# Kernel tuning notes

Hardware: AMD Instinct MI355X
Metric: run time of the kernel (lower is better)

The kernel has to match this reference:

```python
import jax, jax.numpy as jnp
import numpy as np

B, S, D, H = 2, 2048, 1024, 16
DEPTH = D // H
NEG = -1e9

def setup_inputs() -> dict:
    key = jax.random.key(0)
    k = jax.random.split(key, 4)
    return {
        "token_inputs": jax.random.normal(k[0], (B, S, D), dtype=jnp.float32),
        "mask": jnp.zeros((B, 1, 1, S), dtype=jnp.float32),
        "W_qkv": jax.random.normal(k[1], (D, 3 * D), dtype=jnp.float32) * 0.02,
        "b_qkv": jnp.zeros((3 * D,), dtype=jnp.float32),
        "W_out": jax.random.normal(k[2], (D, D), dtype=jnp.float32) * 0.02,
        "b_out": jnp.zeros((D,), dtype=jnp.float32),
    }

def reference(token_inputs, mask, W_qkv, b_qkv, W_out, b_out):
    # fused QKV projection
    qkv = token_inputs @ W_qkv + b_qkv                       # [B,S,3D]
    q, k, v = jnp.split(qkv, 3, axis=-1)                     # [B,S,D] each
    # split heads -> [B,H,S,depth]
    split = lambda x: x.reshape(B, S, H, DEPTH).transpose(0, 2, 1, 3)
    q, k, v = split(q), split(k), split(v)
    # causal additive mask: 0 on/below diagonal, -1e9 above
    causal = (1.0 - jnp.tril(jnp.ones((S, S), dtype=jnp.float32))) * NEG
    full_mask = mask + causal                                # [B,1,S,S]
    # scaled dot-product attention
    scores = jnp.einsum('bhqd,bhkd->bhqk', q, k) / jnp.sqrt(jnp.float32(DEPTH))
    scores = scores + full_mask
    attn = jax.nn.softmax(scores, axis=-1)                   # [B,H,S,S]
    ctx = jnp.einsum('bhqk,bhkd->bhqd', attn, v)             # [B,H,S,depth]
    # merge heads and final projection
    ctx = ctx.transpose(0, 2, 1, 3).reshape(B, S, D)
    return ctx @ W_out + b_out
```

## Files before the change

kernel.cpp:

```cpp
#include <hip/hip_runtime.h>
#include <hip/hip_bf16.h>

#define B_ 2
#define S_ 2048
#define D_ 1024
#define H_ 16
#define DEPTH_ 64

typedef __attribute__((ext_vector_type(4))) float f32x4;
typedef __attribute__((ext_vector_type(16))) float f32x16;
typedef __attribute__((ext_vector_type(8))) short bf16x8;
typedef const __attribute__((address_space(1))) unsigned int gu32;
typedef __attribute__((address_space(3))) unsigned int lu32;

__device__ __forceinline__ void gload_lds16(const void* g, void* l) {
  __builtin_amdgcn_global_load_lds((gu32*)g, (lu32*)l, 16, 0, 0);
}

__device__ __forceinline__ short f2bf(float f) {
  union { float f; unsigned u; } v; v.f = f;
  return (short)((v.u + 0x7FFFu + ((v.u >> 16) & 1u)) >> 16);
}
__device__ __forceinline__ unsigned pk2(float lo, float hi) {
  unsigned r;
  asm("v_cvt_pk_bf16_f32 %0, %1, %2" : "=v"(r) : "v"(lo), "v"(hi));
  return r;
}

__global__ __launch_bounds__(256) void cast_kernel(const float* __restrict__ in,
                                                   short* __restrict__ out, int n4) {
  int i = blockIdx.x * 256 + threadIdx.x;
  if (i < n4) {
    const float4 v = reinterpret_cast<const float4*>(in)[i];
    short2 a, b;
    *reinterpret_cast<unsigned*>(&a) = pk2(v.x, v.y);
    *reinterpret_cast<unsigned*>(&b) = pk2(v.z, v.w);
    reinterpret_cast<short4*>(out)[i] = make_short4(a.x, a.y, b.x, b.y);
  }
}

__global__ __launch_bounds__(256) void transpose_cast_kernel(const float* __restrict__ W,
                                                             short* __restrict__ WT,
                                                             int K, int N) {
  __shared__ short tile[32][33];
  int n0 = blockIdx.x * 32, k0 = blockIdx.y * 32;
  int tx = threadIdx.x, ty = threadIdx.y;
#pragma unroll
  for (int j = 0; j < 4; ++j)
    tile[ty + 8 * j][tx] = f2bf(W[(size_t)(k0 + ty + 8 * j) * N + n0 + tx]);
  __syncthreads();
#pragma unroll
  for (int j = 0; j < 4; ++j)
    WT[(size_t)(n0 + ty + 8 * j) * K + k0 + tx] = tile[tx][ty + 8 * j];
}

template <int EPI, int BM>
__global__ __launch_bounds__(512) void gemm_bt_kernel(
    const short* __restrict__ A, const short* __restrict__ BT,
    const float* __restrict__ bias,
    short* __restrict__ Qh, short* __restrict__ Kh, short* __restrict__ VTt,
    float* __restrict__ Out, int M, int N, int K) {
  constexpr int MI = BM / 64;
  constexpr int ASZ = BM * 32;
  constexpr int BSZ = 128 * 32;
  __shared__ short smem[2 * ASZ + 2 * BSZ];
  const int bm = blockIdx.y * BM, bn = blockIdx.x * 128;
  const int tid = threadIdx.x;
  const int w = tid >> 6, lane = tid & 63;
  const int wr = w >> 1, wc = w & 1;
  const int lr = lane & 15, lg = lane >> 4;
  const int s_r = lane >> 2, s_c = (lane & 3) * 8;
  f32x4 acc[MI][4] = {};
  const int nk = K >> 5;

  auto stage = [&](int buf, int kt) {
    short* Asb = smem + (buf ? ASZ : 0);
    short* Bsb = smem + 2 * ASZ + (buf ? BSZ : 0);
    if (BM == 128 || w < 4)
      gload_lds16(&A[(size_t)(bm + 16 * w + s_r) * K + kt * 32 + s_c], &Asb[16 * w * 32]);
    gload_lds16(&BT[(size_t)(bn + 16 * w + s_r) * K + kt * 32 + s_c], &Bsb[16 * w * 32]);
  };

  stage(0, 0);
  __syncthreads();
  int cur = 0;
  for (int kt = 0; kt < nk; ++kt) {
    if (kt + 1 < nk) stage(cur ^ 1, kt + 1);
    const short* Asb = smem + (cur ? ASZ : 0);
    const short* Bsb = smem + 2 * ASZ + (cur ? BSZ : 0);
    bf16x8 af[MI], bfr[4];
#pragma unroll
    for (int mi = 0; mi < MI; ++mi)
      af[mi] = *reinterpret_cast<const bf16x8*>(&Asb[((BM / 4) * wr + 16 * mi + lr) * 32 + 8 * lg]);
#pragma unroll
    for (int ni = 0; ni < 4; ++ni)
      bfr[ni] = *reinterpret_cast<const bf16x8*>(&Bsb[(64 * wc + 16 * ni + lr) * 32 + 8 * lg]);
#pragma unroll
    for (int mi = 0; mi < MI; ++mi)
#pragma unroll
      for (int ni = 0; ni < 4; ++ni)
        acc[mi][ni] = __builtin_amdgcn_mfma_f32_16x16x32_bf16(af[mi], bfr[ni], acc[mi][ni], 0, 0, 0);
    __syncthreads();
    cur ^= 1;
  }

  if constexpr (EPI == 0) {
    if (bn >= 2 * D_) {
      __syncthreads();
      short* vt = smem;
#pragma unroll
      for (int mi = 0; mi < MI; ++mi)
#pragma unroll
        for (int ni = 0; ni < 4; ++ni)
#pragma unroll
          for (int r = 0; r < 4; r += 2) {
            int row_local = (BM / 4) * wr + 16 * mi + 4 * lg + r;
            int col_local = 64 * wc + 16 * ni + lr;
            float bv = bias[bn + col_local];
            unsigned u = pk2(acc[mi][ni][r] + bv, acc[mi][ni][r + 1] + bv);
            int rsw = row_local ^ ((col_local & 7) << 3);
            *reinterpret_cast<unsigned*>(&vt[col_local * 128 + rsw]) = u;
          }
      __syncthreads();
      const int b = bm >> 11, sbase = bm & (S_ - 1);
#pragma unroll
      for (int p = 0; p < 4; ++p) {
        int slot = 512 * p + tid;
        int vrow = slot >> 4, seg = slot & 15;
        int dd_col = bn - 2 * D_ + vrow;
        int hh = dd_col >> 6, dd = dd_col & 63;
        int csw = (seg * 8) ^ ((vrow & 7) << 3);
        short* dst = &VTt[((size_t)(b * H_ + hh) * DEPTH_ + dd) * S_ + sbase + seg * 8];
        *reinterpret_cast<bf16x8*>(dst) = *reinterpret_cast<const bf16x8*>(&vt[vrow * 128 + csw]);
      }
    } else {
#pragma unroll
      for (int mi = 0; mi < MI; ++mi)
#pragma unroll
        for (int ni = 0; ni < 4; ++ni)
#pragma unroll
          for (int r = 0; r < 4; ++r) {
            int row = bm + (BM / 4) * wr + 16 * mi + 4 * lg + r;
            int col = bn + 64 * wc + 16 * ni + lr;
            float v = acc[mi][ni][r] + bias[col];
            int b = row >> 11, s = row & (S_ - 1);
            int which = col >> 10, cm = col & (D_ - 1);
            int hh = cm >> 6, dd = cm & 63;
            short bv = f2bf(v);
            size_t bh = (size_t)(b * H_ + hh);
            if (which == 0) Qh[(bh * S_ + s) * DEPTH_ + dd] = bv;
            else            Kh[(bh * S_ + s) * DEPTH_ + dd] = bv;
          }
    }
  } else {
#pragma unroll
    for (int mi = 0; mi < MI; ++mi)
#pragma unroll
      for (int ni = 0; ni < 4; ++ni)
#pragma unroll
        for (int r = 0; r < 4; ++r) {
          int row = bm + (BM / 4) * wr + 16 * mi + 4 * lg + r;
          int col = bn + 64 * wc + 16 * ni + lr;
          Out[(size_t)row * N + col] = acc[mi][ni][r] + bias[col];
        }
  }
}

__global__ __launch_bounds__(256, 4) void attn_kernel(
    const short* __restrict__ Qh, const short* __restrict__ Kh,
    const short* __restrict__ VTt, const float* __restrict__ mask,
    short* __restrict__ ctx) {
  constexpr float SC = 0.125f * 1.44269504f;
  __shared__ short smem[16384];
  const int bid = blockIdx.x;
  const int j = bid >> 5, g = j & 7, rr = j >> 3;
  const int qt = (rr == 0) ? 31 - g : (rr == 1) ? 16 + g : (rr == 2) ? 15 - g : g;
  const int bh = bid & 31;
  const int b = bh >> 4, h = bh & 15;
  const short* Qp = Qh + (size_t)bh * S_ * DEPTH_;
  const short* Kp = Kh + (size_t)bh * S_ * DEPTH_;
  const short* Vp = VTt + (size_t)bh * DEPTH_ * S_;
  const int tid = threadIdx.x;
  const int w = tid >> 6, lane = tid & 63;
  const int sw = w & 1, ch = w >> 1;
  const int lq = lane & 31, hi = lane >> 5;
  const int q0w = qt * 64 + sw * 32;
  const int scs = 8 * ((lane & 7) ^ ((lane >> 3) & 7));
  const int srw = lane >> 3;
  short* Ksc = smem + ch * 8192;
  short* Vsc = Ksc + 4096;

  bf16x8 qf[4];
#pragma unroll
  for (int ksd = 0; ksd < 4; ++ksd)
    qf[ksd] = *reinterpret_cast<const bf16x8*>(&Qp[(size_t)(q0w + lq) * DEPTH_ + 16 * ksd + 8 * hi]);

  bf16x8 ones = {};
  if (hi == 0) ones[0] = (short)0x3F80;

  f32x16 acc0 = {}, acc1 = {};
  float m_run = -1e30f, l_run = 0.f;

  const int nt = qt + 1;
  const int nh = (nt + 1) >> 1;
  for (int i = 0; i < nh; ++i) {
    const int kt = ch ? (nh + i) : i;
    const bool valid = kt < nt;
    const int k0 = kt * 64;
    __syncthreads();
    if (valid) {
#pragma unroll
      for (int jj = 0; jj < 4; ++jj) {
        const int brow = sw * 32 + jj * 8;
        gload_lds16(&Kp[(size_t)(k0 + brow + srw) * DEPTH_ + scs], &Ksc[brow * 64]);
        gload_lds16(&Vp[(size_t)(brow + srw) * S_ + k0 + scs], &Vsc[brow * 64]);
      }
    }
    __syncthreads();
    if (!valid) continue;

    f32x16 sc[2] = {{}, {}};
#pragma unroll
    for (int h2 = 0; h2 < 2; ++h2) {
#pragma unroll
      for (int ksd = 0; ksd < 4; ++ksd) {
        const int row = h2 * 32 + lq;
        const int col = (16 * ksd + 8 * hi) ^ ((row & 7) * 8);
        bf16x8 kf = *reinterpret_cast<const bf16x8*>(&Ksc[row * 64 + col]);
        sc[h2] = __builtin_amdgcn_mfma_f32_32x32x16_bf16(kf, qf[ksd], sc[h2], 0, 0, 0);
      }
      float mv = mask[(size_t)b * S_ + k0 + h2 * 32 + lq];
      bf16x8 maf = {};
      if (hi == 0) maf[0] = f2bf(8.f * mv);
      sc[h2] = __builtin_amdgcn_mfma_f32_32x32x16_bf16(maf, ones, sc[h2], 0, 0, 0);
    }
    if (kt == nt - 1) {
      const int qg = q0w + lq;
#pragma unroll
      for (int h2 = 0; h2 < 2; ++h2)
#pragma unroll
        for (int r = 0; r < 16; ++r) {
          int kvg = k0 + (r & 3) + 8 * (r >> 2) + 4 * hi + 32 * h2;
          if (kvg > qg) sc[h2][r] = -1e30f;
        }
    }
    float mx = fmaxf(sc[0][0], sc[0][1]);
#pragma unroll
    for (int r = 2; r < 16; ++r) mx = fmaxf(mx, sc[0][r]);
#pragma unroll
    for (int r = 0; r < 16; ++r) mx = fmaxf(mx, sc[1][r]);
    mx = fmaxf(mx, __shfl_xor(mx, 32));
    const float m_tile = mx * SC;
    if (__any(m_tile > m_run + 8.f)) {
      const float m_new = fmaxf(m_run, m_tile);
      const float corr = exp2f(m_run - m_new);
      m_run = m_new;
      l_run *= corr;
#pragma unroll
      for (int r = 0; r < 16; ++r) { acc0[r] *= corr; acc1[r] *= corr; }
    }
    float su = 0.f;
#pragma unroll
    for (int h2 = 0; h2 < 2; ++h2)
#pragma unroll
      for (int r = 0; r < 16; ++r) {
        float p = exp2f(fmaf(sc[h2][r], SC, -m_run));
        sc[h2][r] = p;
        su += p;
      }
    su += __shfl_xor(su, 32);
    l_run += su;

#pragma unroll
    for (int h2 = 0; h2 < 2; ++h2) {
#pragma unroll
      for (int ks = 0; ks < 2; ++ks) {
        const int rb = 8 * ks;
        unsigned a = pk2(sc[h2][rb + 0], sc[h2][rb + 1]);
        unsigned bq = pk2(sc[h2][rb + 2], sc[h2][rb + 3]);
        unsigned c = pk2(sc[h2][rb + 4], sc[h2][rb + 5]);
        unsigned d = pk2(sc[h2][rb + 6], sc[h2][rb + 7]);
        unsigned sa = __shfl_xor((int)a, 32), sb = __shfl_xor((int)bq, 32);
        unsigned sx = __shfl_xor((int)c, 32), sy = __shfl_xor((int)d, 32);
        union { unsigned u[4]; bf16x8 v; } pf;
        pf.u[0] = hi ? sx : a;
        pf.u[1] = hi ? sy : bq;
        pf.u[2] = hi ? c : sa;
        pf.u[3] = hi ? d : sb;
#pragma unroll
        for (int dh = 0; dh < 2; ++dh) {
          const int row = dh * 32 + lq;
          const int col = (32 * h2 + 16 * ks + 8 * hi) ^ ((row & 7) * 8);
          bf16x8 vf = *reinterpret_cast<const bf16x8*>(&Vsc[row * 64 + col]);
          if (dh == 0) acc0 = __builtin_amdgcn_mfma_f32_32x32x16_bf16(vf, pf.v, acc0, 0, 0, 0);
          else         acc1 = __builtin_amdgcn_mfma_f32_32x32x16_bf16(vf, pf.v, acc1, 0, 0, 0);
        }
      }
    }
  }

  __syncthreads();
  float* F  = (float*)smem;
  float* ML = (float*)(smem + 8192);
  short* ob = smem + 8704;
  if (ch == 1) {
    float* dst = F + ((size_t)sw * 64 + lane) * 32;
#pragma unroll
    for (int r = 0; r < 16; ++r) { dst[r] = acc0[r]; dst[16 + r] = acc1[r]; }
    ML[(sw * 64 + lane) * 2 + 0] = m_run;
    ML[(sw * 64 + lane) * 2 + 1] = l_run;
  }
  __syncthreads();
  if (ch == 0) {
    const float* src = F + ((size_t)sw * 64 + lane) * 32;
    const float m1 = ML[(sw * 64 + lane) * 2 + 0];
    const float l1 = ML[(sw * 64 + lane) * 2 + 1];
    const float mM = fmaxf(m_run, m1);
    const float f0 = exp2f(m_run - mM), f1 = exp2f(m1 - mM);
    const float rl = 1.f / (l_run * f0 + l1 * f1);
    const float g0 = f0 * rl, g1 = f1 * rl;
#pragma unroll
    for (int r = 0; r < 16; ++r) {
      acc0[r] = acc0[r] * g0 + src[r] * g1;
      acc1[r] = acc1[r] * g0 + src[16 + r] * g1;
    }
#pragma unroll
    for (int dh = 0; dh < 2; ++dh) {
      const f32x16& Aa = dh ? acc1 : acc0;
#pragma unroll
      for (int gg = 0; gg < 4; ++gg)
#pragma unroll
        for (int p = 0; p < 2; ++p) {
          int r0 = 4 * gg + 2 * p;
          int d0 = 2 * p + 8 * gg + 4 * hi + 32 * dh;
          unsigned u = pk2(Aa[r0], Aa[r0 + 1]);
          *reinterpret_cast<unsigned*>(&ob[(sw * 32 + lq) * 72 + d0]) = u;
        }
    }
  }
  __syncthreads();
  {
    const int row = tid >> 2, seg = tid & 3;
    short* dst = ctx + ((size_t)b * S_ + qt * 64 + row) * D_ + h * 64 + seg * 16;
    const short* srcp = &ob[row * 72 + seg * 16];
    *reinterpret_cast<bf16x8*>(dst) = *reinterpret_cast<const bf16x8*>(srcp);
    *reinterpret_cast<bf16x8*>(dst + 8) = *reinterpret_cast<const bf16x8*>(srcp + 8);
  }
}

extern "C" void kernel_launch(void* const* d_in, const int* in_sizes, int n_in,
                              void* d_out, int out_size, void* d_ws, size_t ws_size,
                              hipStream_t stream) {
  const float* X    = (const float*)d_in[0];
  const float* mask = (const float*)d_in[1];
  const float* Wqkv = (const float*)d_in[2];
  const float* bqkv = (const float*)d_in[3];
  const float* Wout = (const float*)d_in[4];
  const float* bout = (const float*)d_in[5];
  float* Out = (float*)d_out;

  short* ws    = (short*)d_ws;
  short* Xb    = ws;
  short* WqkvT = Xb + (size_t)4096 * 1024;
  short* WoutT = WqkvT + (size_t)3072 * 1024;
  short* Qh    = WoutT + (size_t)1024 * 1024;
  short* Kh    = Qh + (size_t)B_ * H_ * S_ * DEPTH_;
  short* VTt   = Kh + (size_t)B_ * H_ * S_ * DEPTH_;
  short* ctx   = VTt + (size_t)B_ * H_ * S_ * DEPTH_;

  cast_kernel<<<4096, 256, 0, stream>>>(X, Xb, (4096 * 1024) / 4);
  transpose_cast_kernel<<<dim3(96, 32), dim3(32, 8), 0, stream>>>(Wqkv, WqkvT, 1024, 3072);
  transpose_cast_kernel<<<dim3(32, 32), dim3(32, 8), 0, stream>>>(Wout, WoutT, 1024, 1024);
  gemm_bt_kernel<0, 128><<<dim3(24, 32), 512, 0, stream>>>(Xb, WqkvT, bqkv, Qh, Kh, VTt, nullptr,
                                                           4096, 3072, 1024);
  attn_kernel<<<1024, 256, 0, stream>>>(Qh, Kh, VTt, mask, ctx);
  gemm_bt_kernel<1, 64><<<dim3(8, 64), 512, 0, stream>>>(ctx, WoutT, bout, nullptr, nullptr, nullptr,
                                                         Out, 4096, 1024, 1024);
}
```

Before: 116.8 us.

## Halve attention block to 32 query rows and 32-key tiles with 2048 blocks

Rewrites the attention kernel so each 128-thread block handles 32 query rows instead of 64, iterating over 32-wide key/value tiles split between two waves. The grid grows to 2048 blocks, launched heaviest-first instead of with the previous balanced pairing, and the V shared-memory layout and swizzle are reworked for 32-column tiles. The aim is finer causal granularity (less masked work on diagonal tiles), more parallelism and a smaller LDS footprint. In exchange, K/V tiles are reloaded for each 32-row query block, roughly doubling K/V traffic, and there are more barriers per unit of work.

```diff
diff --git a/kernel.cpp b/kernel.cpp
--- a/kernel.cpp
+++ b/kernel.cpp
@@ -166,29 +166,29 @@
   }
 }
 
-__global__ __launch_bounds__(256, 4) void attn_kernel(
+__global__ __launch_bounds__(128, 4) void attn_kernel(
     const short* __restrict__ Qh, const short* __restrict__ Kh,
     const short* __restrict__ VTt, const float* __restrict__ mask,
     short* __restrict__ ctx) {
   constexpr float SC = 0.125f * 1.44269504f;
-  __shared__ short smem[16384];
+  __shared__ short smem[8192];
   const int bid = blockIdx.x;
-  const int j = bid >> 5, g = j & 7, rr = j >> 3;
-  const int qt = (rr == 0) ? 31 - g : (rr == 1) ? 16 + g : (rr == 2) ? 15 - g : g;
+  const int ss = 63 - (bid >> 5);
   const int bh = bid & 31;
   const int b = bh >> 4, h = bh & 15;
   const short* Qp = Qh + (size_t)bh * S_ * DEPTH_;
   const short* Kp = Kh + (size_t)bh * S_ * DEPTH_;
   const short* Vp = VTt + (size_t)bh * DEPTH_ * S_;
   const int tid = threadIdx.x;
-  const int w = tid >> 6, lane = tid & 63;
-  const int sw = w & 1, ch = w >> 1;
+  const int ch = tid >> 6, lane = tid & 63;
   const int lq = lane & 31, hi = lane >> 5;
-  const int q0w = qt * 64 + sw * 32;
-  const int scs = 8 * ((lane & 7) ^ ((lane >> 3) & 7));
+  const int q0w = ss * 32;
   const int srw = lane >> 3;
-  short* Ksc = smem + ch * 8192;
-  short* Vsc = Ksc + 4096;
+  const int scs = 8 * ((lane & 7) ^ srw);
+  const int vrl = lane >> 2;
+  const int vcs = 8 * ((lane & 3) ^ (vrl & 3));
+  short* Ksc = smem + ch * 4096;
+  short* Vsc = Ksc + 2048;
 
   bf16x8 qf[4];
 #pragma unroll
@@ -201,54 +201,50 @@
   f32x16 acc0 = {}, acc1 = {};
   float m_run = -1e30f, l_run = 0.f;
 
-  const int nt = qt + 1;
+  const int nt = ss + 1;
   const int nh = (nt + 1) >> 1;
   for (int i = 0; i < nh; ++i) {
     const int kt = ch ? (nh + i) : i;
     const bool valid = kt < nt;
-    const int k0 = kt * 64;
+    const int k0 = kt * 32;
     __syncthreads();
     if (valid) {
 #pragma unroll
-      for (int jj = 0; jj < 4; ++jj) {
-        const int brow = sw * 32 + jj * 8;
-        gload_lds16(&Kp[(size_t)(k0 + brow + srw) * DEPTH_ + scs], &Ksc[brow * 64]);
-        gload_lds16(&Vp[(size_t)(brow + srw) * S_ + k0 + scs], &Vsc[brow * 64]);
+      for (int j = 0; j < 4; ++j) {
+        gload_lds16(&Kp[(size_t)(k0 + j * 8 + srw) * DEPTH_ + scs], &Ksc[j * 8 * 64]);
+        gload_lds16(&Vp[(size_t)(j * 16 + vrl) * S_ + k0 + vcs], &Vsc[j * 16 * 32]);
       }
     }
     __syncthreads();
     if (!valid) continue;
 
-    f32x16 sc[2] = {{}, {}};
-#pragma unroll
-    for (int h2 = 0; h2 < 2; ++h2) {
-#pragma unroll
-      for (int ksd = 0; ksd < 4; ++ksd) {
-        const int row = h2 * 32 + lq;
-        const int col = (16 * ksd + 8 * hi) ^ ((row & 7) * 8);
-        bf16x8 kf = *reinterpret_cast<const bf16x8*>(&Ksc[row * 64 + col]);
-        sc[h2] = __builtin_amdgcn_mfma_f32_32x32x16_bf16(kf, qf[ksd], sc[h2], 0, 0, 0);
-      }
-      float mv = mask[(size_t)b * S_ + k0 + h2 * 32 + lq];
+    f32x16 sc = {};
+#pragma unroll
+    for (int ksd = 0; ksd < 4; ++ksd) {
+      bf16x8 kf = *reinterpret_cast<const bf16x8*>(
+          &Ksc[lq * 64 + ((16 * ksd + 8 * hi) ^ ((lq & 7) * 8))]);
+      sc = __builtin_amdgcn_mfma_f32_32x32x16_bf16(kf, qf[ksd], sc, 0, 0, 0);
+    }
+    {
+      float mv = mask[(size_t)b * S_ + k0 + lq];
       bf16x8 maf = {};
       if (hi == 0) maf[0] = f2bf(8.f * mv);
-      sc[h2] = __builtin_amdgcn_mfma_f32_32x32x16_bf16(maf, ones, sc[h2], 0, 0, 0);
+      sc = __builtin_amdgcn_mfma_f32_32x32x16_bf16(maf, ones, sc, 0, 0, 0);
     }
     if (kt == nt - 1) {
       const int qg = q0w + lq;
 #pragma unroll
-      for (int h2 = 0; h2 < 2; ++h2)
-#pragma unroll
-        for (int r = 0; r < 16; ++r) {
-          int kvg = k0 + (r & 3) + 8 * (r >> 2) + 4 * hi + 32 * h2;
-          if (kvg > qg) sc[h2][r] = -1e30f;
-        }
-    }
-    float mx = fmaxf(sc[0][0], sc[0][1]);
-#pragma unroll
-    for (int r = 2; r < 16; ++r) mx = fmaxf(mx, sc[0][r]);
-#pragma unroll
-    for (int r = 0; r < 16; ++r) mx = fmaxf(mx, sc[1][r]);
+      for (int r = 0; r < 16; ++r) {
+        int kvg = k0 + (r & 3) + 8 * (r >> 2) + 4 * hi;
+        if (kvg > qg) sc[r] = -1e30f;
+      }
+    }
+    float t8[8];
+#pragma unroll
+    for (int r = 0; r < 8; ++r) t8[r] = fmaxf(sc[r], sc[r + 8]);
+#pragma unroll
+    for (int r = 0; r < 4; ++r) t8[r] = fmaxf(t8[r], t8[r + 4]);
+    float mx = fmaxf(fmaxf(t8[0], t8[1]), fmaxf(t8[2], t8[3]));
     mx = fmaxf(mx, __shfl_xor(mx, 32));
     const float m_tile = mx * SC;
     if (__any(m_tile > m_run + 8.f)) {
@@ -259,62 +255,58 @@
 #pragma unroll
       for (int r = 0; r < 16; ++r) { acc0[r] *= corr; acc1[r] *= corr; }
     }
-    float su = 0.f;
-#pragma unroll
-    for (int h2 = 0; h2 < 2; ++h2)
-#pragma unroll
-      for (int r = 0; r < 16; ++r) {
-        float p = exp2f(fmaf(sc[h2][r], SC, -m_run));
-        sc[h2][r] = p;
-        su += p;
-      }
+    float s8[8];
+#pragma unroll
+    for (int r = 0; r < 16; ++r) sc[r] = exp2f(fmaf(sc[r], SC, -m_run));
+#pragma unroll
+    for (int r = 0; r < 8; ++r) s8[r] = sc[r] + sc[r + 8];
+#pragma unroll
+    for (int r = 0; r < 4; ++r) s8[r] = s8[r] + s8[r + 4];
+    float su = (s8[0] + s8[1]) + (s8[2] + s8[3]);
     su += __shfl_xor(su, 32);
     l_run += su;
 
 #pragma unroll
-    for (int h2 = 0; h2 < 2; ++h2) {
-#pragma unroll
-      for (int ks = 0; ks < 2; ++ks) {
-        const int rb = 8 * ks;
-        unsigned a = pk2(sc[h2][rb + 0], sc[h2][rb + 1]);
-        unsigned bq = pk2(sc[h2][rb + 2], sc[h2][rb + 3]);
-        unsigned c = pk2(sc[h2][rb + 4], sc[h2][rb + 5]);
-        unsigned d = pk2(sc[h2][rb + 6], sc[h2][rb + 7]);
-        unsigned sa = __shfl_xor((int)a, 32), sb = __shfl_xor((int)bq, 32);
-        unsigned sx = __shfl_xor((int)c, 32), sy = __shfl_xor((int)d, 32);
-        union { unsigned u[4]; bf16x8 v; } pf;
-        pf.u[0] = hi ? sx : a;
-        pf.u[1] = hi ? sy : bq;
-        pf.u[2] = hi ? c : sa;
-        pf.u[3] = hi ? d : sb;
-#pragma unroll
-        for (int dh = 0; dh < 2; ++dh) {
-          const int row = dh * 32 + lq;
-          const int col = (32 * h2 + 16 * ks + 8 * hi) ^ ((row & 7) * 8);
-          bf16x8 vf = *reinterpret_cast<const bf16x8*>(&Vsc[row * 64 + col]);
-          if (dh == 0) acc0 = __builtin_amdgcn_mfma_f32_32x32x16_bf16(vf, pf.v, acc0, 0, 0, 0);
-          else         acc1 = __builtin_amdgcn_mfma_f32_32x32x16_bf16(vf, pf.v, acc1, 0, 0, 0);
-        }
+    for (int ks = 0; ks < 2; ++ks) {
+      const int j0 = 2 * ks, j1 = 2 * ks + 1;
+      unsigned ra0 = pk2(sc[4 * j0 + 0], sc[4 * j0 + 1]);
+      unsigned rb0 = pk2(sc[4 * j0 + 2], sc[4 * j0 + 3]);
+      unsigned ra1 = pk2(sc[4 * j1 + 0], sc[4 * j1 + 1]);
+      unsigned rb1 = pk2(sc[4 * j1 + 2], sc[4 * j1 + 3]);
+      unsigned pa0 = __shfl_xor((int)ra0, 32), pb0 = __shfl_xor((int)rb0, 32);
+      unsigned pa1 = __shfl_xor((int)ra1, 32), pb1 = __shfl_xor((int)rb1, 32);
+      union { unsigned u[4]; bf16x8 v; } pf;
+      pf.u[0] = hi ? pa1 : ra0;
+      pf.u[1] = hi ? pb1 : rb0;
+      pf.u[2] = hi ? ra1 : pa0;
+      pf.u[3] = hi ? rb1 : pb0;
+#pragma unroll
+      for (int dh = 0; dh < 2; ++dh) {
+        const int row = dh * 32 + lq;
+        bf16x8 vf = *reinterpret_cast<const bf16x8*>(
+            &Vsc[row * 32 + (((2 * ks + hi) ^ (row & 3)) * 8)]);
+        if (dh == 0) acc0 = __builtin_amdgcn_mfma_f32_32x32x16_bf16(vf, pf.v, acc0, 0, 0, 0);
+        else         acc1 = __builtin_amdgcn_mfma_f32_32x32x16_bf16(vf, pf.v, acc1, 0, 0, 0);
       }
     }
   }
 
   __syncthreads();
   float* F  = (float*)smem;
-  float* ML = (float*)(smem + 8192);
-  short* ob = smem + 8704;
+  float* ML = (float*)(smem + 4096);
+  short* ob = smem + 4096 + 256;
   if (ch == 1) {
-    float* dst = F + ((size_t)sw * 64 + lane) * 32;
+    float* dst = F + (size_t)lane * 32;
 #pragma unroll
     for (int r = 0; r < 16; ++r) { dst[r] = acc0[r]; dst[16 + r] = acc1[r]; }
-    ML[(sw * 64 + lane) * 2 + 0] = m_run;
-    ML[(sw * 64 + lane) * 2 + 1] = l_run;
+    ML[lane * 2 + 0] = m_run;
+    ML[lane * 2 + 1] = l_run;
   }
   __syncthreads();
   if (ch == 0) {
-    const float* src = F + ((size_t)sw * 64 + lane) * 32;
-    const float m1 = ML[(sw * 64 + lane) * 2 + 0];
-    const float l1 = ML[(sw * 64 + lane) * 2 + 1];
+    const float* src = F + (size_t)lane * 32;
+    const float m1 = ML[lane * 2 + 0];
+    const float l1 = ML[lane * 2 + 1];
     const float mM = fmaxf(m_run, m1);
     const float f0 = exp2f(m_run - mM), f1 = exp2f(m1 - mM);
     const float rl = 1.f / (l_run * f0 + l1 * f1);
@@ -334,14 +326,14 @@
           int r0 = 4 * gg + 2 * p;
           int d0 = 2 * p + 8 * gg + 4 * hi + 32 * dh;
           unsigned u = pk2(Aa[r0], Aa[r0 + 1]);
-          *reinterpret_cast<unsigned*>(&ob[(sw * 32 + lq) * 72 + d0]) = u;
+          *reinterpret_cast<unsigned*>(&ob[lq * 72 + d0]) = u;
         }
     }
   }
   __syncthreads();
   {
     const int row = tid >> 2, seg = tid & 3;
-    short* dst = ctx + ((size_t)b * S_ + qt * 64 + row) * D_ + h * 64 + seg * 16;
+    short* dst = ctx + ((size_t)b * S_ + q0w + row) * D_ + h * 64 + seg * 16;
     const short* srcp = &ob[row * 72 + seg * 16];
     *reinterpret_cast<bf16x8*>(dst) = *reinterpret_cast<const bf16x8*>(srcp);
     *reinterpret_cast<bf16x8*>(dst + 8) = *reinterpret_cast<const bf16x8*>(srcp + 8);
@@ -373,7 +365,7 @@
   transpose_cast_kernel<<<dim3(32, 32), dim3(32, 8), 0, stream>>>(Wout, WoutT, 1024, 1024);
   gemm_bt_kernel<0, 128><<<dim3(24, 32), 512, 0, stream>>>(Xb, WqkvT, bqkv, Qh, Kh, VTt, nullptr,
                                                            4096, 3072, 1024);
-  attn_kernel<<<1024, 256, 0, stream>>>(Qh, Kh, VTt, mask, ctx);
+  attn_kernel<<<2048, 128, 0, stream>>>(Qh, Kh, VTt, mask, ctx);
   gemm_bt_kernel<1, 64><<<dim3(8, 64), 512, 0, stream>>>(ctx, WoutT, bout, nullptr, nullptr, nullptr,
                                                          Out, 4096, 1024, 1024);
 }
```

New measurement: 126.4 us. +8.2%, slower.

## Restructure attention into 2-wave blocks with per-wave K/V prefetch pipelining

Applied to the files above, without the earlier changes.

The attention kernel now uses 128-thread blocks covering 32 query rows instead of 256-thread blocks covering 64. Each of the two waves owns a private LDS tile and a contiguous half of the KV range. Block-wide __syncthreads in the KV loop are replaced by per-wave vmcnt/lgkmcnt waits, and the next K and V tiles are issued asynchronously as soon as the current ones have been consumed, so loads overlap the softmax and PV matmuls. It also adds s_setprio around MFMA groups, tree-shaped max/sum reductions and a simpler heavy-first block ordering. The cost is that the finer query granularity loads each K/V tile twice as often from global memory.

```diff
diff --git a/kernel.cpp b/kernel.cpp
--- a/kernel.cpp
+++ b/kernel.cpp
@@ -26,6 +26,10 @@
   asm("v_cvt_pk_bf16_f32 %0, %1, %2" : "=v"(r) : "v"(lo), "v"(hi));
   return r;
 }
+#define WAIT_VM0() do { asm volatile("s_waitcnt vmcnt(0)" ::: "memory"); \
+                        __builtin_amdgcn_sched_barrier(0); } while (0)
+#define WAIT_LG0() do { asm volatile("s_waitcnt lgkmcnt(0)" ::: "memory"); \
+                        __builtin_amdgcn_sched_barrier(0); } while (0)
 
 __global__ __launch_bounds__(256) void cast_kernel(const float* __restrict__ in,
                                                    short* __restrict__ out, int n4) {
@@ -166,30 +170,41 @@
   }
 }
 
-__global__ __launch_bounds__(256, 4) void attn_kernel(
+__global__ __launch_bounds__(128, 2) void attn_kernel(
     const short* __restrict__ Qh, const short* __restrict__ Kh,
     const short* __restrict__ VTt, const float* __restrict__ mask,
     short* __restrict__ ctx) {
   constexpr float SC = 0.125f * 1.44269504f;
   __shared__ short smem[16384];
   const int bid = blockIdx.x;
-  const int j = bid >> 5, g = j & 7, rr = j >> 3;
-  const int qt = (rr == 0) ? 31 - g : (rr == 1) ? 16 + g : (rr == 2) ? 15 - g : g;
+  const int ss = 63 - (bid >> 5);
   const int bh = bid & 31;
   const int b = bh >> 4, h = bh & 15;
   const short* Qp = Qh + (size_t)bh * S_ * DEPTH_;
   const short* Kp = Kh + (size_t)bh * S_ * DEPTH_;
   const short* Vp = VTt + (size_t)bh * DEPTH_ * S_;
   const int tid = threadIdx.x;
-  const int w = tid >> 6, lane = tid & 63;
-  const int sw = w & 1, ch = w >> 1;
+  const int ch = tid >> 6, lane = tid & 63;
   const int lq = lane & 31, hi = lane >> 5;
-  const int q0w = qt * 64 + sw * 32;
-  const int scs = 8 * ((lane & 7) ^ ((lane >> 3) & 7));
+  const int q0w = ss * 32;
   const int srw = lane >> 3;
+  const int scs = 8 * ((lane & 7) ^ srw);
   short* Ksc = smem + ch * 8192;
   short* Vsc = Ksc + 4096;
 
+  auto issueK = [&](int kt) {
+    const int k0 = kt * 64;
+#pragma unroll
+    for (int j = 0; j < 8; ++j)
+      gload_lds16(&Kp[(size_t)(k0 + j * 8 + srw) * DEPTH_ + scs], &Ksc[j * 8 * 64]);
+  };
+  auto issueV = [&](int kt) {
+    const int k0 = kt * 64;
+#pragma unroll
+    for (int j = 0; j < 8; ++j)
+      gload_lds16(&Vp[(size_t)(j * 8 + srw) * S_ + k0 + scs], &Vsc[j * 8 * 64]);
+  };
+
   bf16x8 qf[4];
 #pragma unroll
   for (int ksd = 0; ksd < 4; ++ksd)
@@ -201,120 +216,130 @@
   f32x16 acc0 = {}, acc1 = {};
   float m_run = -1e30f, l_run = 0.f;
 
-  const int nt = qt + 1;
+  const int nt = (ss >> 1) + 1;
   const int nh = (nt + 1) >> 1;
-  for (int i = 0; i < nh; ++i) {
-    const int kt = ch ? (nh + i) : i;
-    const bool valid = kt < nt;
-    const int k0 = kt * 64;
-    __syncthreads();
-    if (valid) {
-#pragma unroll
-      for (int jj = 0; jj < 4; ++jj) {
-        const int brow = sw * 32 + jj * 8;
-        gload_lds16(&Kp[(size_t)(k0 + brow + srw) * DEPTH_ + scs], &Ksc[brow * 64]);
-        gload_lds16(&Vp[(size_t)(brow + srw) * S_ + k0 + scs], &Vsc[brow * 64]);
+  const int my0 = ch ? nh : 0;
+  const int myn = ch ? (nt - nh) : nh;
+
+  if (myn > 0) {
+    issueK(my0);
+    issueV(my0);
+    for (int i = 0; i < myn; ++i) {
+      const int kt = my0 + i;
+      const int k0 = kt * 64;
+      WAIT_VM0();
+
+      f32x16 sc[2] = {{}, {}};
+      __builtin_amdgcn_s_setprio(1);
+#pragma unroll
+      for (int h2 = 0; h2 < 2; ++h2)
+#pragma unroll
+        for (int ksd = 0; ksd < 4; ++ksd) {
+          const int row = h2 * 32 + lq;
+          bf16x8 kf = *reinterpret_cast<const bf16x8*>(
+              &Ksc[row * 64 + ((16 * ksd + 8 * hi) ^ ((row & 7) * 8))]);
+          sc[h2] = __builtin_amdgcn_mfma_f32_32x32x16_bf16(kf, qf[ksd], sc[h2], 0, 0, 0);
+        }
+      __builtin_amdgcn_s_setprio(0);
+      WAIT_LG0();
+      if (i + 1 < myn) issueK(kt + 1);
+
+#pragma unroll
+      for (int h2 = 0; h2 < 2; ++h2) {
+        float mv = mask[(size_t)b * S_ + k0 + h2 * 32 + lq];
+        bf16x8 maf = {};
+        if (hi == 0) maf[0] = f2bf(8.f * mv);
+        sc[h2] = __builtin_amdgcn_mfma_f32_32x32x16_bf16(maf, ones, sc[h2], 0, 0, 0);
       }
-    }
-    __syncthreads();
-    if (!valid) continue;
-
-    f32x16 sc[2] = {{}, {}};
-#pragma unroll
-    for (int h2 = 0; h2 < 2; ++h2) {
-#pragma unroll
-      for (int ksd = 0; ksd < 4; ++ksd) {
-        const int row = h2 * 32 + lq;
-        const int col = (16 * ksd + 8 * hi) ^ ((row & 7) * 8);
-        bf16x8 kf = *reinterpret_cast<const bf16x8*>(&Ksc[row * 64 + col]);
-        sc[h2] = __builtin_amdgcn_mfma_f32_32x32x16_bf16(kf, qf[ksd], sc[h2], 0, 0, 0);
+      if (kt == nt - 1) {
+        const int qg = q0w + lq;
+#pragma unroll
+        for (int h2 = 0; h2 < 2; ++h2)
+#pragma unroll
+          for (int r = 0; r < 16; ++r) {
+            int kvg = k0 + (r & 3) + 8 * (r >> 2) + 4 * hi + 32 * h2;
+            if (kvg > qg) sc[h2][r] = -1e30f;
+          }
       }
-      float mv = mask[(size_t)b * S_ + k0 + h2 * 32 + lq];
-      bf16x8 maf = {};
-      if (hi == 0) maf[0] = f2bf(8.f * mv);
-      sc[h2] = __builtin_amdgcn_mfma_f32_32x32x16_bf16(maf, ones, sc[h2], 0, 0, 0);
-    }
-    if (kt == nt - 1) {
-      const int qg = q0w + lq;
+      float t8[8];
+#pragma unroll
+      for (int r = 0; r < 8; ++r) t8[r] = fmaxf(fmaxf(sc[0][r], sc[0][r + 8]),
+                                                fmaxf(sc[1][r], sc[1][r + 8]));
+#pragma unroll
+      for (int r = 0; r < 4; ++r) t8[r] = fmaxf(t8[r], t8[r + 4]);
+      float mx = fmaxf(fmaxf(t8[0], t8[1]), fmaxf(t8[2], t8[3]));
+      mx = fmaxf(mx, __shfl_xor(mx, 32));
+      const float m_tile = mx * SC;
+      if (__any(m_tile > m_run + 8.f)) {
+        const float m_new = fmaxf(m_run, m_tile);
+        const float corr = exp2f(m_run - m_new);
+        m_run = m_new;
+        l_run *= corr;
+#pragma unroll
+        for (int r = 0; r < 16; ++r) { acc0[r] *= corr; acc1[r] *= corr; }
+      }
+      float s8[8];
 #pragma unroll
       for (int h2 = 0; h2 < 2; ++h2)
 #pragma unroll
-        for (int r = 0; r < 16; ++r) {
-          int kvg = k0 + (r & 3) + 8 * (r >> 2) + 4 * hi + 32 * h2;
-          if (kvg > qg) sc[h2][r] = -1e30f;
-        }
-    }
-    float mx = fmaxf(sc[0][0], sc[0][1]);
-#pragma unroll
-    for (int r = 2; r < 16; ++r) mx = fmaxf(mx, sc[0][r]);
-#pragma unroll
-    for (int r = 0; r < 16; ++r) mx = fmaxf(mx, sc[1][r]);
-    mx = fmaxf(mx, __shfl_xor(mx, 32));
-    const float m_tile = mx * SC;
-    if (__any(m_tile > m_run + 8.f)) {
-      const float m_new = fmaxf(m_run, m_tile);
-      const float corr = exp2f(m_run - m_new);
-      m_run = m_new;
-      l_run *= corr;
-#pragma unroll
-      for (int r = 0; r < 16; ++r) { acc0[r] *= corr; acc1[r] *= corr; }
-    }
-    float su = 0.f;
-#pragma unroll
-    for (int h2 = 0; h2 < 2; ++h2)
-#pragma unroll
-      for (int r = 0; r < 16; ++r) {
-        float p = exp2f(fmaf(sc[h2][r], SC, -m_run));
-        sc[h2][r] = p;
-        su += p;
-      }
-    su += __shfl_xor(su, 32);
-    l_run += su;
-
-#pragma unroll
-    for (int h2 = 0; h2 < 2; ++h2) {
-#pragma unroll
-      for (int ks = 0; ks < 2; ++ks) {
-        const int rb = 8 * ks;
-        unsigned a = pk2(sc[h2][rb + 0], sc[h2][rb + 1]);
-        unsigned bq = pk2(sc[h2][rb + 2], sc[h2][rb + 3]);
-        unsigned c = pk2(sc[h2][rb + 4], sc[h2][rb + 5]);
-        unsigned d = pk2(sc[h2][rb + 6], sc[h2][rb + 7]);
-        unsigned sa = __shfl_xor((int)a, 32), sb = __shfl_xor((int)bq, 32);
-        unsigned sx = __shfl_xor((int)c, 32), sy = __shfl_xor((int)d, 32);
-        union { unsigned u[4]; bf16x8 v; } pf;
-        pf.u[0] = hi ? sx : a;
-        pf.u[1] = hi ? sy : bq;
-        pf.u[2] = hi ? c : sa;
-        pf.u[3] = hi ? d : sb;
-#pragma unroll
-        for (int dh = 0; dh < 2; ++dh) {
-          const int row = dh * 32 + lq;
-          const int col = (32 * h2 + 16 * ks + 8 * hi) ^ ((row & 7) * 8);
-          bf16x8 vf = *reinterpret_cast<const bf16x8*>(&Vsc[row * 64 + col]);
-          if (dh == 0) acc0 = __builtin_amdgcn_mfma_f32_32x32x16_bf16(vf, pf.v, acc0, 0, 0, 0);
-          else         acc1 = __builtin_amdgcn_mfma_f32_32x32x16_bf16(vf, pf.v, acc1, 0, 0, 0);
+        for (int r = 0; r < 16; ++r) sc[h2][r] = exp2f(fmaf(sc[h2][r], SC, -m_run));
+#pragma unroll
+      for (int r = 0; r < 8; ++r) s8[r] = (sc[0][r] + sc[0][r + 8]) + (sc[1][r] + sc[1][r + 8]);
+#pragma unroll
+      for (int r = 0; r < 4; ++r) s8[r] = s8[r] + s8[r + 4];
+      float su = (s8[0] + s8[1]) + (s8[2] + s8[3]);
+      su += __shfl_xor(su, 32);
+      l_run += su;
+
+#pragma unroll
+      for (int h2 = 0; h2 < 2; ++h2) {
+#pragma unroll
+        for (int ks = 0; ks < 2; ++ks) {
+          const int rb = 8 * ks;
+          unsigned a = pk2(sc[h2][rb + 0], sc[h2][rb + 1]);
+          unsigned bq = pk2(sc[h2][rb + 2], sc[h2][rb + 3]);
+          unsigned c = pk2(sc[h2][rb + 4], sc[h2][rb + 5]);
+          unsigned d = pk2(sc[h2][rb + 6], sc[h2][rb + 7]);
+          unsigned sa = __shfl_xor((int)a, 32), sb = __shfl_xor((int)bq, 32);
+          unsigned sx = __shfl_xor((int)c, 32), sy = __shfl_xor((int)d, 32);
+          union { unsigned u[4]; bf16x8 v; } pf;
+          pf.u[0] = hi ? sx : a;
+          pf.u[1] = hi ? sy : bq;
+          pf.u[2] = hi ? c : sa;
+          pf.u[3] = hi ? d : sb;
+          __builtin_amdgcn_s_setprio(1);
+#pragma unroll
+          for (int dh = 0; dh < 2; ++dh) {
+            const int row = dh * 32 + lq;
+            bf16x8 vf = *reinterpret_cast<const bf16x8*>(
+                &Vsc[row * 64 + ((32 * h2 + 16 * ks + 8 * hi) ^ ((row & 7) * 8))]);
+            if (dh == 0) acc0 = __builtin_amdgcn_mfma_f32_32x32x16_bf16(vf, pf.v, acc0, 0, 0, 0);
+            else         acc1 = __builtin_amdgcn_mfma_f32_32x32x16_bf16(vf, pf.v, acc1, 0, 0, 0);
+          }
+          __builtin_amdgcn_s_setprio(0);
         }
       }
+      WAIT_LG0();
+      if (i + 1 < myn) issueV(kt + 1);
     }
   }
 
   __syncthreads();
   float* F  = (float*)smem;
-  float* ML = (float*)(smem + 8192);
-  short* ob = smem + 8704;
+  float* ML = (float*)(smem + 4096);
+  short* ob = smem + 4608;
   if (ch == 1) {
-    float* dst = F + ((size_t)sw * 64 + lane) * 32;
+    float* dst = F + (size_t)lane * 32;
 #pragma unroll
     for (int r = 0; r < 16; ++r) { dst[r] = acc0[r]; dst[16 + r] = acc1[r]; }
-    ML[(sw * 64 + lane) * 2 + 0] = m_run;
-    ML[(sw * 64 + lane) * 2 + 1] = l_run;
+    ML[lane * 2 + 0] = m_run;
+    ML[lane * 2 + 1] = l_run;
   }
   __syncthreads();
   if (ch == 0) {
-    const float* src = F + ((size_t)sw * 64 + lane) * 32;
-    const float m1 = ML[(sw * 64 + lane) * 2 + 0];
-    const float l1 = ML[(sw * 64 + lane) * 2 + 1];
+    const float* src = F + (size_t)lane * 32;
+    const float m1 = ML[lane * 2 + 0];
+    const float l1 = ML[lane * 2 + 1];
     const float mM = fmaxf(m_run, m1);
     const float f0 = exp2f(m_run - mM), f1 = exp2f(m1 - mM);
     const float rl = 1.f / (l_run * f0 + l1 * f1);
@@ -334,14 +359,14 @@
           int r0 = 4 * gg + 2 * p;
           int d0 = 2 * p + 8 * gg + 4 * hi + 32 * dh;
           unsigned u = pk2(Aa[r0], Aa[r0 + 1]);
-          *reinterpret_cast<unsigned*>(&ob[(sw * 32 + lq) * 72 + d0]) = u;
+          *reinterpret_cast<unsigned*>(&ob[lq * 72 + d0]) = u;
         }
     }
   }
   __syncthreads();
   {
     const int row = tid >> 2, seg = tid & 3;
-    short* dst = ctx + ((size_t)b * S_ + qt * 64 + row) * D_ + h * 64 + seg * 16;
+    short* dst = ctx + ((size_t)b * S_ + q0w + row) * D_ + h * 64 + seg * 16;
     const short* srcp = &ob[row * 72 + seg * 16];
     *reinterpret_cast<bf16x8*>(dst) = *reinterpret_cast<const bf16x8*>(srcp);
     *reinterpret_cast<bf16x8*>(dst + 8) = *reinterpret_cast<const bf16x8*>(srcp + 8);
@@ -373,7 +398,7 @@
   transpose_cast_kernel<<<dim3(32, 32), dim3(32, 8), 0, stream>>>(Wout, WoutT, 1024, 1024);
   gemm_bt_kernel<0, 128><<<dim3(24, 32), 512, 0, stream>>>(Xb, WqkvT, bqkv, Qh, Kh, VTt, nullptr,
                                                            4096, 3072, 1024);
-  attn_kernel<<<1024, 256, 0, stream>>>(Qh, Kh, VTt, mask, ctx);
+  attn_kernel<<<2048, 128, 0, stream>>>(Qh, Kh, VTt, mask, ctx);
   gemm_bt_kernel<1, 64><<<dim3(8, 64), 512, 0, stream>>>(ctx, WoutT, bout, nullptr, nullptr, nullptr,
                                                          Out, 4096, 1024, 1024);
 }
```

Result: slower. 128.0 us (+9.5%).
